# Kernel optimization log

Hardware: AMD Instinct MI355X
Metric: run time of the kernel (lower is better)

## Reference

```python
import jax, jax.numpy as jnp
import numpy as np

T, B, D = 2048, 8, 1024
INIT_ALPHA_BIAS = 2.0


def setup_inputs() -> dict:
    key = jax.random.key(0)
    k1, k2, k3, k4 = jax.random.split(key, 4)
    xav = float(np.sqrt(6.0 / (D + D)))  # xavier_uniform bound
    return {
        "x": jax.random.normal(k1, (T, B, D), dtype=jnp.float32),
        "h0": jax.random.normal(k2, (B, D), dtype=jnp.float32),
        "W_alpha": jax.random.uniform(k3, (D, D), jnp.float32, -xav, xav),
        "b_alpha": jnp.full((D,), INIT_ALPHA_BIAS, dtype=jnp.float32),
        "W_v": jax.random.uniform(k4, (D, D), jnp.float32, -xav, xav),
        "b_v": jnp.zeros((D,), dtype=jnp.float32),
    }


def reference(x, h0, W_alpha, b_alpha, W_v, b_v):
    # Gates/values for all timesteps at once (batched GEMMs): [T, B, D]
    alpha = jax.nn.sigmoid(jnp.einsum("tbd,ed->tbe", x, W_alpha) + b_alpha)
    v = jnp.einsum("tbd,ed->tbe", x, W_v) + b_v

    def step(h_prev, av):
        a_t, v_t = av
        h_new = a_t * h_prev + (1.0 - a_t) * v_t
        out_t = h_new * jax.nn.silu(h_new)
        return h_new, (h_new, out_t)

    _, (hs, output) = jax.lax.scan(step, h0, (alpha, v))
    h = jnp.concatenate([h0[None], hs], axis=0)  # [T+1, B, D]
    return output, h
```

## Files before the change

### kernel.cpp

```cpp
#include <hip/hip_runtime.h>
#include <hip/hip_bf16.h>

#define T_DIM 2048
#define B_DIM 8
#define D_DIM 1024
#define M_DIM (T_DIM * B_DIM)
#define K_DIM D_DIM
#define NW_DIM (2 * D_DIM)
#define NCH (B_DIM * D_DIM)
#define NCH4 (NCH / 4)
#define CHUNKS 64
#define CHUNK_LEN 32

typedef __attribute__((ext_vector_type(8))) short bf16x8;
typedef __attribute__((ext_vector_type(4))) float f32x4;

__device__ __forceinline__ unsigned short bf16_rne(float f) {
    unsigned u = __float_as_uint(f);
    unsigned r = u + 0x7fffu + ((u >> 16) & 1u);
    return (unsigned short)(r >> 16);
}

__device__ __forceinline__ float sigmoidf(float z) {
    return 1.0f / (1.0f + __expf(-z));
}

__device__ __forceinline__ void load_lds16(const void* g, void* l) {
    __builtin_amdgcn_global_load_lds(
        (const __attribute__((address_space(1))) void*)g,
        (__attribute__((address_space(3))) void*)l,
        16, 0, 0);
}

__global__ void f32_to_bf16_kernel(const float4* __restrict__ in,
                                   ushort4* __restrict__ out, int n4) {
    int i = blockIdx.x * blockDim.x + threadIdx.x;
    if (i < n4) {
        float4 f = in[i];
        ushort4 o;
        o.x = bf16_rne(f.x);
        o.y = bf16_rne(f.y);
        o.z = bf16_rne(f.z);
        o.w = bf16_rne(f.w);
        out[i] = o;
    }
}

__global__ void conv_weights_kernel(const float4* __restrict__ Wa,
                                    const float4* __restrict__ Wv,
                                    ushort4* __restrict__ Wcat) {
    const int half4 = D_DIM * D_DIM / 4;
    int i = blockIdx.x * blockDim.x + threadIdx.x;
    float4 f = (i < half4) ? Wa[i] : Wv[i - half4];
    ushort4 o;
    o.x = bf16_rne(f.x);
    o.y = bf16_rne(f.y);
    o.z = bf16_rne(f.z);
    o.w = bf16_rne(f.w);
    Wcat[i] = o;
}

#define MMA_QUAD(IB)                                                        \
    _Pragma("unroll") for (int i = 0; i < 4; ++i)                           \
    _Pragma("unroll") for (int j = 0; j < 4; ++j)                           \
        acc[(IB) + i][j] = __builtin_amdgcn_mfma_f32_16x16x32_bf16(         \
            af[i], bf[j], acc[(IB) + i][j], 0, 0, 0);

__global__ __launch_bounds__(512, 2) void gemm_fused_kernel(
    const unsigned short* __restrict__ A,
    const unsigned short* __restrict__ W,
    const float* __restrict__ ba,
    const float* __restrict__ bv,
    float* __restrict__ alpha_dst,
    float* __restrict__ v_dst) {
    extern __shared__ __attribute__((aligned(16))) char smem[];

    const int tid = threadIdx.x;
    const int lane = tid & 63;
    const int w = tid >> 6;
    const int wm = w >> 2;
    const int wn = w & 3;
    const int quad = lane >> 4;
    const int l16 = lane & 15;

    const int bid = blockIdx.x;
    const int swz = (bid & 7) * 64 + (bid >> 3);
    const int bx = swz & 7;
    const int by = swz >> 3;
    const int bm = by * 256;
    const int bn = bx * 256;

    const int vsw = (((l16 & 1) << 2) | quad) ^ (l16 >> 1);
    const int rdA = wm * 8192 + (l16 >> 1) * 128 + vsw * 16;
    const int rdB = wn * 4096 + (l16 >> 1) * 128 + vsw * 16;

    const int p = lane & 7;
    const int hl = lane >> 3;
    const int vp = p ^ hl;
    const int qsrc = vp & 3;
    const int rb = (vp >> 2) & 1;
    const int r0 = 16 * (2 * w + 0) + 2 * hl + rb;
    const int r1 = 16 * (2 * w + 1) + 2 * hl + rb;
    const char* Ab = (const char*)A;
    const char* Wb = (const char*)W;
    const size_t offA0 = (size_t)(bm + r0) * 2048 + (size_t)qsrc * 16;
    const size_t offA1 = (size_t)(bm + r1) * 2048 + (size_t)qsrc * 16;
    const size_t offB0 = (size_t)(bn + r0) * 2048 + (size_t)qsrc * 16;
    const size_t offB1 = (size_t)(bn + r1) * 2048 + (size_t)qsrc * 16;
    const int lds0 = (2 * w + 0) * 1024;
    const int lds1 = (2 * w + 1) * 1024;

    f32x4 acc[8][4];
    bf16x8 af[4], bf[4];
    {
        f32x4 zero = {0.f, 0.f, 0.f, 0.f};
#pragma unroll
        for (int i = 0; i < 8; ++i)
#pragma unroll
            for (int j = 0; j < 4; ++j) acc[i][j] = zero;
    }

    auto stage_a = [&](int buf, int ts) {
        char* base = smem + (buf << 15);
        load_lds16(Ab + offA0 + (size_t)ts * 64, base + lds0);
        load_lds16(Ab + offA1 + (size_t)ts * 64, base + lds1);
    };
    auto stage_b = [&](int buf, int ts) {
        char* base = smem + (buf << 15) + 16384;
        load_lds16(Wb + offB0 + (size_t)ts * 64, base + lds0);
        load_lds16(Wb + offB1 + (size_t)ts * 64, base + lds1);
    };
    auto read_a = [&](int buf, int ib) {
        const char* la = smem + (buf << 15);
#pragma unroll
        for (int i = 0; i < 4; ++i)
            af[i] = *(const bf16x8*)(la + rdA + (ib + i) * 1024);
    };
    auto read_b = [&](int buf) {
        const char* lb = smem + (buf << 15) + 16384;
#pragma unroll
        for (int j = 0; j < 4; ++j)
            bf[j] = *(const bf16x8*)(lb + rdB + j * 1024);
    };

    auto phaseA = [&](int t, bool do_stage) {
        const int buf = t & 3;
        read_a(buf, 0);
        read_b(buf);
        if (do_stage) stage_a((t + 2) & 3, t + 2);
        __builtin_amdgcn_s_barrier();
        asm volatile("s_waitcnt lgkmcnt(0)" ::: "memory");
        __builtin_amdgcn_sched_barrier(0);
        __builtin_amdgcn_s_setprio(1);
        MMA_QUAD(0)
        __builtin_amdgcn_s_setprio(0);
        __builtin_amdgcn_s_barrier();
    };
    auto phaseB = [&](int t, bool do_stage, int vm) {
        const int buf = t & 3;
        read_a(buf, 4);
        if (do_stage) stage_b((t + 2) & 3, t + 2);
        if (vm == 4) asm volatile("s_waitcnt vmcnt(4)" ::: "memory");
        else if (vm == 0) asm volatile("s_waitcnt vmcnt(0)" ::: "memory");
        __builtin_amdgcn_s_barrier();
        asm volatile("s_waitcnt lgkmcnt(0)" ::: "memory");
        __builtin_amdgcn_sched_barrier(0);
        __builtin_amdgcn_s_setprio(1);
        MMA_QUAD(4)
        __builtin_amdgcn_s_setprio(0);
        __builtin_amdgcn_s_barrier();
    };

    stage_a(0, 0); stage_b(0, 0);
    stage_a(1, 1); stage_b(1, 1);
    asm volatile("s_waitcnt vmcnt(4)" ::: "memory");
    __builtin_amdgcn_s_barrier();

    for (int t = 0; t < 30; ++t) {
        phaseA(t, true);
        phaseB(t, true, 4);
    }
    phaseA(30, false);
    phaseB(30, false, 0);
    phaseA(31, false);
    phaseB(31, false, -1);

    const bool is_alpha = (bn < D_DIM);
    float* __restrict__ dst = is_alpha ? alpha_dst : v_dst;
    const float* __restrict__ bias = is_alpha ? ba : bv;
    const int nb = bn - (is_alpha ? 0 : D_DIM);
#pragma unroll
    for (int j = 0; j < 4; ++j) {
        const int n = nb + wn * 64 + j * 16 + l16;
        const float bias_n = bias[n];
#pragma unroll
        for (int i = 0; i < 8; ++i) {
            const int m0 = bm + wm * 128 + i * 16 + quad * 4;
#pragma unroll
            for (int r = 0; r < 4; ++r) {
                float val = acc[i][j][r] + bias_n;
                if (is_alpha) val = sigmoidf(val);
                dst[(size_t)(m0 + r) * D_DIM + n] = val;
            }
        }
    }
}


__global__ __launch_bounds__(256) void scan_phase1_kernel(
    const float4* __restrict__ alpha,
    const float4* __restrict__ v,
    float4* __restrict__ P,
    float4* __restrict__ Q) {
    const int j4 = blockIdx.x * 256 + threadIdx.x;
    const int c = blockIdx.y;
    float4 Pr = {1.f, 1.f, 1.f, 1.f};
    float4 Qr = {0.f, 0.f, 0.f, 0.f};
    size_t base = (size_t)c * CHUNK_LEN * NCH4 + j4;
#pragma unroll 4
    for (int t = 0; t < CHUNK_LEN; ++t) {
        float4 a = alpha[base + (size_t)t * NCH4];
        float4 vv = v[base + (size_t)t * NCH4];
        Pr.x *= a.x; Pr.y *= a.y; Pr.z *= a.z; Pr.w *= a.w;
        Qr.x = a.x * Qr.x + (1.f - a.x) * vv.x;
        Qr.y = a.y * Qr.y + (1.f - a.y) * vv.y;
        Qr.z = a.z * Qr.z + (1.f - a.z) * vv.z;
        Qr.w = a.w * Qr.w + (1.f - a.w) * vv.w;
    }
    P[(size_t)c * NCH4 + j4] = Pr;
    Q[(size_t)c * NCH4 + j4] = Qr;
}

__global__ __launch_bounds__(256) void scan_phase2_kernel(
    const float4* __restrict__ P, const float4* __restrict__ Q,
    const float4* __restrict__ h0,
    float4* __restrict__ Hc) {
    const int j4 = blockIdx.x * 256 + threadIdx.x;
    float4 h = h0[j4];
#pragma unroll 8
    for (int c = 0; c < CHUNKS; ++c) {
        Hc[(size_t)c * NCH4 + j4] = h;
        float4 p = P[(size_t)c * NCH4 + j4];
        float4 q = Q[(size_t)c * NCH4 + j4];
        h.x = p.x * h.x + q.x;
        h.y = p.y * h.y + q.y;
        h.z = p.z * h.z + q.z;
        h.w = p.w * h.w + q.w;
    }
}

__global__ __launch_bounds__(256) void scan_phase3_kernel(
    float4* __restrict__ alpha_out,
    float4* __restrict__ v_h,
    const float4* __restrict__ Hc) {
    const int j4 = blockIdx.x * 256 + threadIdx.x;
    const int c = blockIdx.y;
    float4 h = Hc[(size_t)c * NCH4 + j4];
    size_t base = (size_t)c * CHUNK_LEN * NCH4 + j4;
#pragma unroll 4
    for (int t = 0; t < CHUNK_LEN; ++t) {
        float4 a = alpha_out[base + (size_t)t * NCH4];
        float4 vv = v_h[base + (size_t)t * NCH4];
        h.x = a.x * h.x + (1.f - a.x) * vv.x;
        h.y = a.y * h.y + (1.f - a.y) * vv.y;
        h.z = a.z * h.z + (1.f - a.z) * vv.z;
        h.w = a.w * h.w + (1.f - a.w) * vv.w;
        float4 o;
        o.x = h.x * h.x * sigmoidf(h.x);
        o.y = h.y * h.y * sigmoidf(h.y);
        o.z = h.z * h.z * sigmoidf(h.z);
        o.w = h.w * h.w * sigmoidf(h.w);
        alpha_out[base + (size_t)t * NCH4] = o;
        v_h[base + (size_t)t * NCH4] = h;
    }
}

extern "C" void kernel_launch(void* const* d_in, const int* in_sizes, int n_in,
                              void* d_out, int out_size, void* d_ws, size_t ws_size,
                              hipStream_t stream) {
    const float* x  = (const float*)d_in[0];
    const float* h0 = (const float*)d_in[1];
    const float* Wa = (const float*)d_in[2];
    const float* ba = (const float*)d_in[3];
    const float* Wv = (const float*)d_in[4];
    const float* bv = (const float*)d_in[5];

    float* out = (float*)d_out;
    float* hbase = out + (size_t)T_DIM * NCH;
    float* alpha = out;
    float* vbuf = hbase + NCH;

    char* ws = (char*)d_ws;
    unsigned short* xb   = (unsigned short*)ws;
    unsigned short* Wcat = (unsigned short*)(ws + 33554432);
    float* P  = (float*)(ws + 37748736);
    float* Q  = (float*)(ws + 39845888);
    float* Hc = (float*)(ws + 41943040);

    static bool attr_done = false;
    if (!attr_done) {
        hipFuncSetAttribute(reinterpret_cast<const void*>(gemm_fused_kernel),
                            hipFuncAttributeMaxDynamicSharedMemorySize, 131072);
        attr_done = true;
    }

    f32_to_bf16_kernel<<<(M_DIM * K_DIM / 4) / 256, 256, 0, stream>>>(
        (const float4*)x, (ushort4*)xb, M_DIM * K_DIM / 4);
    conv_weights_kernel<<<(2 * D_DIM * D_DIM / 4) / 256, 256, 0, stream>>>(
        (const float4*)Wa, (const float4*)Wv, (ushort4*)Wcat);

    gemm_fused_kernel<<<512, 512, 131072, stream>>>(xb, Wcat, ba, bv, alpha, vbuf);

    hipMemcpyAsync(hbase, h0, (size_t)NCH * sizeof(float),
                   hipMemcpyDeviceToDevice, stream);

    dim3 sgrid(NCH4 / 256, CHUNKS);
    scan_phase1_kernel<<<sgrid, 256, 0, stream>>>(
        (const float4*)alpha, (const float4*)vbuf, (float4*)P, (float4*)Q);
    scan_phase2_kernel<<<NCH4 / 256, 256, 0, stream>>>(
        (const float4*)P, (const float4*)Q, (const float4*)h0, (float4*)Hc);
    scan_phase3_kernel<<<sgrid, 256, 0, stream>>>(
        (float4*)alpha, (float4*)vbuf, (const float4*)Hc);
}
```

Baseline: 327.4 us.

## Deepen GEMM prefetch to three stages, merge conversions, widen scan phase 2

```diff
diff --git a/kernel.cpp b/kernel.cpp
--- a/kernel.cpp
+++ b/kernel.cpp
@@ -32,32 +32,34 @@
         16, 0, 0);
 }
 
-__global__ void f32_to_bf16_kernel(const float4* __restrict__ in,
-                                   ushort4* __restrict__ out, int n4) {
-    int i = blockIdx.x * blockDim.x + threadIdx.x;
-    if (i < n4) {
-        float4 f = in[i];
-        ushort4 o;
-        o.x = bf16_rne(f.x);
-        o.y = bf16_rne(f.y);
-        o.z = bf16_rne(f.z);
-        o.w = bf16_rne(f.w);
-        out[i] = o;
-    }
-}
-
-__global__ void conv_weights_kernel(const float4* __restrict__ Wa,
-                                    const float4* __restrict__ Wv,
-                                    ushort4* __restrict__ Wcat) {
+__global__ __launch_bounds__(256) void convert_all_kernel(
+    const float4* __restrict__ x,
+    const float4* __restrict__ Wa,
+    const float4* __restrict__ Wv,
+    ushort4* __restrict__ xb,
+    ushort4* __restrict__ Wcat) {
+    const int nx4 = M_DIM * K_DIM / 4;
     const int half4 = D_DIM * D_DIM / 4;
-    int i = blockIdx.x * blockDim.x + threadIdx.x;
-    float4 f = (i < half4) ? Wa[i] : Wv[i - half4];
+    int i = blockIdx.x * 256 + threadIdx.x;
+    float4 f;
+    ushort4* __restrict__ dst;
+    int di;
+    if (i < nx4) {
+        f = x[i];
+        dst = xb;
+        di = i;
+    } else {
+        int j = i - nx4;
+        f = (j < half4) ? Wa[j] : Wv[j - half4];
+        dst = Wcat;
+        di = j;
+    }
     ushort4 o;
     o.x = bf16_rne(f.x);
     o.y = bf16_rne(f.y);
     o.z = bf16_rne(f.z);
     o.w = bf16_rne(f.w);
-    Wcat[i] = o;
+    dst[di] = o;
 }
 
 #define MMA_QUAD(IB)                                                        \
@@ -147,8 +149,7 @@
         const int buf = t & 3;
         read_a(buf, 0);
         read_b(buf);
-        if (do_stage) stage_a((t + 2) & 3, t + 2);
-        __builtin_amdgcn_s_barrier();
+        if (do_stage) stage_a((t + 3) & 3, t + 3);
         asm volatile("s_waitcnt lgkmcnt(0)" ::: "memory");
         __builtin_amdgcn_sched_barrier(0);
         __builtin_amdgcn_s_setprio(1);
@@ -159,10 +160,10 @@
     auto phaseB = [&](int t, bool do_stage, int vm) {
         const int buf = t & 3;
         read_a(buf, 4);
-        if (do_stage) stage_b((t + 2) & 3, t + 2);
-        if (vm == 4) asm volatile("s_waitcnt vmcnt(4)" ::: "memory");
+        if (do_stage) stage_b((t + 3) & 3, t + 3);
+        if (vm == 8) asm volatile("s_waitcnt vmcnt(8)" ::: "memory");
+        else if (vm == 4) asm volatile("s_waitcnt vmcnt(4)" ::: "memory");
         else if (vm == 0) asm volatile("s_waitcnt vmcnt(0)" ::: "memory");
-        __builtin_amdgcn_s_barrier();
         asm volatile("s_waitcnt lgkmcnt(0)" ::: "memory");
         __builtin_amdgcn_sched_barrier(0);
         __builtin_amdgcn_s_setprio(1);
@@ -173,13 +174,16 @@
 
     stage_a(0, 0); stage_b(0, 0);
     stage_a(1, 1); stage_b(1, 1);
-    asm volatile("s_waitcnt vmcnt(4)" ::: "memory");
+    stage_a(2, 2); stage_b(2, 2);
+    asm volatile("s_waitcnt vmcnt(8)" ::: "memory");
     __builtin_amdgcn_s_barrier();
 
-    for (int t = 0; t < 30; ++t) {
+    for (int t = 0; t < 29; ++t) {
         phaseA(t, true);
-        phaseB(t, true, 4);
-    }
+        phaseB(t, true, 8);
+    }
+    phaseA(29, false);
+    phaseB(29, false, 4);
     phaseA(30, false);
     phaseB(30, false, 0);
     phaseA(31, false);
@@ -232,20 +236,17 @@
 }
 
 __global__ __launch_bounds__(256) void scan_phase2_kernel(
-    const float4* __restrict__ P, const float4* __restrict__ Q,
-    const float4* __restrict__ h0,
-    float4* __restrict__ Hc) {
-    const int j4 = blockIdx.x * 256 + threadIdx.x;
-    float4 h = h0[j4];
+    const float* __restrict__ P, const float* __restrict__ Q,
+    const float* __restrict__ h0,
+    float* __restrict__ Hc,
+    float* __restrict__ hbase) {
+    const int ch = blockIdx.x * 256 + threadIdx.x;
+    float h = h0[ch];
+    hbase[ch] = h;
 #pragma unroll 8
     for (int c = 0; c < CHUNKS; ++c) {
-        Hc[(size_t)c * NCH4 + j4] = h;
-        float4 p = P[(size_t)c * NCH4 + j4];
-        float4 q = Q[(size_t)c * NCH4 + j4];
-        h.x = p.x * h.x + q.x;
-        h.y = p.y * h.y + q.y;
-        h.z = p.z * h.z + q.z;
-        h.w = p.w * h.w + q.w;
+        Hc[(size_t)c * NCH + ch] = h;
+        h = P[(size_t)c * NCH + ch] * h + Q[(size_t)c * NCH + ch];
     }
 }
 
@@ -304,21 +305,18 @@
         attr_done = true;
     }
 
-    f32_to_bf16_kernel<<<(M_DIM * K_DIM / 4) / 256, 256, 0, stream>>>(
-        (const float4*)x, (ushort4*)xb, M_DIM * K_DIM / 4);
-    conv_weights_kernel<<<(2 * D_DIM * D_DIM / 4) / 256, 256, 0, stream>>>(
-        (const float4*)Wa, (const float4*)Wv, (ushort4*)Wcat);
+    const int nconv = (M_DIM * K_DIM / 4) + (2 * D_DIM * D_DIM / 4);
+    convert_all_kernel<<<nconv / 256, 256, 0, stream>>>(
+        (const float4*)x, (const float4*)Wa, (const float4*)Wv,
+        (ushort4*)xb, (ushort4*)Wcat);
 
     gemm_fused_kernel<<<512, 512, 131072, stream>>>(xb, Wcat, ba, bv, alpha, vbuf);
-
-    hipMemcpyAsync(hbase, h0, (size_t)NCH * sizeof(float),
-                   hipMemcpyDeviceToDevice, stream);
 
     dim3 sgrid(NCH4 / 256, CHUNKS);
     scan_phase1_kernel<<<sgrid, 256, 0, stream>>>(
         (const float4*)alpha, (const float4*)vbuf, (float4*)P, (float4*)Q);
-    scan_phase2_kernel<<<NCH4 / 256, 256, 0, stream>>>(
-        (const float4*)P, (const float4*)Q, (const float4*)h0, (float4*)Hc);
+    scan_phase2_kernel<<<NCH / 256, 256, 0, stream>>>(
+        P, Q, h0, Hc, hbase);
     scan_phase3_kernel<<<sgrid, 256, 0, stream>>>(
         (float4*)alpha, (float4*)vbuf, (const float4*)Hc);
 }
```

Measured after the change: 320.8 us. 1.02x faster.
